# Kernel optimization log

Hardware: AMD Instinct MI355X
Metric: run time of the kernel (lower is better)

The kernel has to match this reference:

```python
import jax, jax.numpy as jnp
import numpy as np

BN_EPS = 1e-5
N_LAYERS = 3


def _mlp_bn(h, w1, b1, g, beta, w2, b2):
    # Linear -> BatchNorm1d (batch stats, training-mode math) -> ReLU -> Linear
    h = h @ w1 + b1
    mu = jnp.mean(h, axis=0)
    var = jnp.var(h, axis=0)
    h = (h - mu) * jax.lax.rsqrt(var + BN_EPS) * g + beta
    h = jax.nn.relu(h)
    return h @ w2 + b2


def setup_inputs() -> dict:
    key = jax.random.key(0)
    ks = jax.random.split(key, 20)
    N, E, XD, ED, H, C, G = 50000, 640000, 64, 16, 128, 10, 512
    L = N_LAYERS
    s = lambda fan: 1.0 / np.sqrt(fan)
    inp = {
        "x": jax.random.normal(ks[0], (N, XD), jnp.float32),
        "edge_attr": jax.random.normal(ks[1], (E, ED), jnp.float32),
        "node_w": jax.random.uniform(ks[2], (XD, H), jnp.float32, -s(XD), s(XD)),
        "node_b": jnp.zeros((H,), jnp.float32),
        "edge_w": jax.random.uniform(ks[3], (ED, H), jnp.float32, -s(ED), s(ED)),
        "edge_b": jnp.zeros((H,), jnp.float32),
        "lin1_w": jax.random.uniform(ks[4], (L, H, H), jnp.float32, -s(H), s(H)),
        "lin1_b": jnp.zeros((L, H), jnp.float32),
        "bn_g": jnp.ones((L, H), jnp.float32),
        "bn_b": jnp.zeros((L, H), jnp.float32),
        "lin2_w": jax.random.uniform(ks[5], (L, H, H), jnp.float32, -s(H), s(H)),
        "lin2_b": jnp.zeros((L, H), jnp.float32),
        "fc_w": jax.random.uniform(ks[6], (H, C), jnp.float32, -s(H), s(H)),
        "fc_b": jnp.zeros((C,), jnp.float32),
        "edge_index": jax.random.randint(ks[7], (2, E), 0, N, jnp.int64),
        "batch": jnp.sort(jax.random.randint(ks[8], (N,), 0, G, jnp.int64)),
        "num_graphs": G,
    }
    return inp


def reference(x, edge_attr, node_w, node_b, edge_w, edge_b, lin1_w, lin1_b,
              bn_g, bn_b, lin2_w, lin2_b, fc_w, fc_b, edge_index, batch, num_graphs):
    N = x.shape[0]
    src, dst = edge_index[0], edge_index[1]
    h = x @ node_w + node_b                      # [N, H] node encoder
    e = edge_attr @ edge_w + edge_b              # [E, H] edge encoder
    for i in range(N_LAYERS):
        # GINEConv: msg = relu(h[src] + e); aggr = segment_sum at dst; out = MLP(h + aggr) (eps=0)
        msg = jax.nn.relu(h[src] + e)            # [E, H]
        aggr = jax.ops.segment_sum(msg, dst, num_segments=N)
        h = _mlp_bn(h + aggr, lin1_w[i], lin1_b[i], bn_g[i], bn_b[i], lin2_w[i], lin2_b[i])
        h = jax.nn.relu(h)                       # dropout p=0 -> identity
    pooled = jax.ops.segment_sum(h, batch, num_segments=num_graphs)  # global_add_pool
    return pooled @ fc_w + fc_b
```

## Files before the change

kernel.cpp:

```cpp
#include <hip/hip_runtime.h>

#define H   128

typedef __attribute__((ext_vector_type(8))) short short8;
typedef __attribute__((ext_vector_type(4))) float f32x4;

__device__ __forceinline__ unsigned int bfr(float f) {
  unsigned int u = __float_as_uint(f);
  return (u + 0x7fffu + ((u >> 16) & 1u)) >> 16;
}
__device__ __forceinline__ float bf_lo(unsigned int d) {
  return __uint_as_float(d << 16);
}
__device__ __forceinline__ float bf_hi(unsigned int d) {
  return __uint_as_float(d & 0xffff0000u);
}

__global__ __launch_bounds__(256) void prep(const int* __restrict__ dst,
    int* __restrict__ cnt, int E, const float* __restrict__ x,
    const float* __restrict__ node_w, const float* __restrict__ node_b,
    unsigned int* __restrict__ h2, int N, const float* __restrict__ lin1_w,
    const float* __restrict__ lin2_w, unsigned short* __restrict__ wp) {
  int gtid = blockIdx.x * 256 + threadIdx.x;
  int GT = gridDim.x * 256;
  for (int e = gtid; e < E; e += GT) atomicAdd(&cnt[dst[e]], 1);
  int lane = threadIdx.x & 63;
  int wg = blockIdx.x * 4 + (threadIdx.x >> 6);
  int NW = gridDim.x * 4;
  int c = lane * 2;
  float b0 = node_b[c], b1 = node_b[c + 1];
  for (int row = wg; row < N; row += NW) {
    const float* xr = x + (size_t)row * 64;
    float a0 = b0, a1 = b1;
#pragma unroll 8
    for (int k = 0; k < 64; ++k) {
      float xk = xr[k];
      float2 wv = *(const float2*)&node_w[k * H + c];
      a0 = fmaf(xk, wv.x, a0);
      a1 = fmaf(xk, wv.y, a1);
    }
    h2[(size_t)row * 64 + lane] = bfr(a0) | (bfr(a1) << 16);
  }
  for (int idx = gtid; idx < 6 * 16384; idx += GT) {
    int j = idx & 7, ln = (idx >> 3) & 63, ct = (idx >> 9) & 7;
    int kt = (idx >> 12) & 3, mat = idx >> 14;
    int l = mat >> 1, which = mat & 1;
    const float* w = (which == 0 ? lin1_w : lin2_w) + (size_t)l * H * H;
    int k = kt * 32 + (ln >> 4) * 8 + j;
    int n = ct * 16 + (ln & 15);
    wp[idx] = (unsigned short)bfr(w[k * H + n]);
  }
}

__global__ __launch_bounds__(256) void block_sum(const int* __restrict__ cnt,
    int* __restrict__ bsum, int N) {
  int t = threadIdx.x;
  int i = blockIdx.x * 256 + t;
  int v = (i < N) ? cnt[i] : 0;
#pragma unroll
  for (int o = 32; o > 0; o >>= 1) v += __shfl_down(v, o, 64);
  __shared__ int wt[4];
  if ((t & 63) == 0) wt[t >> 6] = v;
  __syncthreads();
  if (t == 0) bsum[blockIdx.x] = wt[0] + wt[1] + wt[2] + wt[3];
}

__global__ __launch_bounds__(1024) void scan_bsum(const int* __restrict__ bsum,
    int* __restrict__ bbase, int nb) {
  __shared__ int s[1024];
  int t = threadIdx.x;
  int v = (t < nb) ? bsum[t] : 0;
  s[t] = v;
  __syncthreads();
  for (int o = 1; o < 1024; o <<= 1) {
    int u = (t >= o) ? s[t - o] : 0;
    __syncthreads();
    s[t] += u;
    __syncthreads();
  }
  if (t < nb) bbase[t] = s[t] - v;
}

__global__ __launch_bounds__(256) void scan_pass(const int* __restrict__ cnt,
    const int* __restrict__ bbase, int* __restrict__ off,
    int* __restrict__ cursor, int N) {
  int t = threadIdx.x;
  int i = blockIdx.x * 256 + t;
  int v = (i < N) ? cnt[i] : 0;
  int lane = t & 63;
  int incl = v;
#pragma unroll
  for (int o = 1; o < 64; o <<= 1) {
    int u = __shfl_up(incl, o, 64);
    if (lane >= o) incl += u;
  }
  __shared__ int wtot[4];
  int w = t >> 6;
  if (lane == 63) wtot[w] = incl;
  __syncthreads();
  if (t == 0) {
    int run = 0;
#pragma unroll
    for (int k = 0; k < 4; ++k) { int tmp = wtot[k]; wtot[k] = run; run += tmp; }
  }
  __syncthreads();
  int excl = incl - v + wtot[w] + bbase[blockIdx.x];
  if (i < N) { off[i] = excl; cursor[i] = excl; }
  if (i == N - 1) off[N] = excl + v;
}

__global__ __launch_bounds__(256) void scatter_csr(const int* __restrict__ src,
    const int* __restrict__ dst, int* __restrict__ cursor,
    int2* __restrict__ es, int E) {
  int e = blockIdx.x * 256 + threadIdx.x;
  if (e < E) {
    int pos = atomicAdd(&cursor[dst[e]], 1);
    es[pos] = make_int2(e, src[e]);
  }
}

__global__ __launch_bounds__(256) void aggr_csr(const float* __restrict__ ea,
    const float* __restrict__ ew, const float* __restrict__ eb,
    const int2* __restrict__ es, const int* __restrict__ off,
    const unsigned int* __restrict__ h2, unsigned int* __restrict__ zb,
    int N) {
  int wid = threadIdx.x >> 6, lane = threadIdx.x & 63;
  int n = blockIdx.x * 4 + wid;
  if (n >= N) return;
  int beg = off[n], end = off[n + 1];
  int c = lane * 2;
  float2 wc[16];
#pragma unroll
  for (int k = 0; k < 16; ++k) wc[k] = *(const float2*)&ew[k * H + c];
  float2 bias = *(const float2*)&eb[c];
  float ax = 0.f, ay = 0.f;
  int i = beg;
  for (; i + 4 <= end; i += 4) {
    int2 p0 = es[i], p1 = es[i + 1], p2 = es[i + 2], p3 = es[i + 3];
    int e0 = __builtin_amdgcn_readfirstlane(p0.x);
    int s0 = __builtin_amdgcn_readfirstlane(p0.y);
    int e1 = __builtin_amdgcn_readfirstlane(p1.x);
    int s1 = __builtin_amdgcn_readfirstlane(p1.y);
    int e2 = __builtin_amdgcn_readfirstlane(p2.x);
    int s2 = __builtin_amdgcn_readfirstlane(p2.y);
    int e3 = __builtin_amdgcn_readfirstlane(p3.x);
    int s3 = __builtin_amdgcn_readfirstlane(p3.y);
    unsigned int hv0 = h2[(size_t)s0 * 64 + lane];
    unsigned int hv1 = h2[(size_t)s1 * 64 + lane];
    unsigned int hv2 = h2[(size_t)s2 * 64 + lane];
    unsigned int hv3 = h2[(size_t)s3 * 64 + lane];
    const float* a0 = ea + (size_t)e0 * 16;
    const float* a1 = ea + (size_t)e1 * 16;
    const float* a2 = ea + (size_t)e2 * 16;
    const float* a3 = ea + (size_t)e3 * 16;
    float x0 = bias.x, y0 = bias.y, x1 = bias.x, y1 = bias.y;
    float x2 = bias.x, y2 = bias.y, x3 = bias.x, y3 = bias.y;
#pragma unroll
    for (int k = 0; k < 16; ++k) {
      float a0k = a0[k], a1k = a1[k], a2k = a2[k], a3k = a3[k];
      float2 w = wc[k];
      x0 = fmaf(a0k, w.x, x0); y0 = fmaf(a0k, w.y, y0);
      x1 = fmaf(a1k, w.x, x1); y1 = fmaf(a1k, w.y, y1);
      x2 = fmaf(a2k, w.x, x2); y2 = fmaf(a2k, w.y, y2);
      x3 = fmaf(a3k, w.x, x3); y3 = fmaf(a3k, w.y, y3);
    }
    ax += fmaxf(x0 + bf_lo(hv0), 0.f) + fmaxf(x1 + bf_lo(hv1), 0.f) +
          fmaxf(x2 + bf_lo(hv2), 0.f) + fmaxf(x3 + bf_lo(hv3), 0.f);
    ay += fmaxf(y0 + bf_hi(hv0), 0.f) + fmaxf(y1 + bf_hi(hv1), 0.f) +
          fmaxf(y2 + bf_hi(hv2), 0.f) + fmaxf(y3 + bf_hi(hv3), 0.f);
  }
  for (; i < end; ++i) {
    int2 p0 = es[i];
    int e0 = __builtin_amdgcn_readfirstlane(p0.x);
    int s0 = __builtin_amdgcn_readfirstlane(p0.y);
    unsigned int hv0 = h2[(size_t)s0 * 64 + lane];
    const float* a0 = ea + (size_t)e0 * 16;
    float x0 = bias.x, y0 = bias.y;
#pragma unroll
    for (int k = 0; k < 16; ++k) {
      float a0k = a0[k];
      x0 = fmaf(a0k, wc[k].x, x0);
      y0 = fmaf(a0k, wc[k].y, y0);
    }
    ax += fmaxf(x0 + bf_lo(hv0), 0.f);
    ay += fmaxf(y0 + bf_hi(hv0), 0.f);
  }
  unsigned int hn = h2[(size_t)n * 64 + lane];
  zb[(size_t)n * 64 + lane] =
      bfr(bf_lo(hn) + ax) | (bfr(bf_hi(hn) + ay) << 16);
}

__global__ __launch_bounds__(256) void mlp1m(const unsigned short* __restrict__ zb,
    const unsigned short* __restrict__ wp, const float* __restrict__ b1,
    float* __restrict__ tout, float* __restrict__ sum,
    float* __restrict__ sumsq, int N) {
  int tid = threadIdx.x;
  int wave = tid >> 6, lane = tid & 63;
  int q = lane >> 4, m = lane & 15;
  int r0 = blockIdx.x * 64 + wave * 16;
  f32x4 acc[8];
#pragma unroll
  for (int ct = 0; ct < 8; ++ct) acc[ct] = (f32x4){0.f, 0.f, 0.f, 0.f};
#pragma unroll
  for (int kt = 0; kt < 4; ++kt) {
    short8 a = *(const short8*)(zb + (size_t)(r0 + m) * H + kt * 32 + q * 8);
#pragma unroll
    for (int ct = 0; ct < 8; ++ct) {
      short8 b = *(const short8*)(wp + ((size_t)(kt * 8 + ct) * 64 + lane) * 8);
      acc[ct] = __builtin_amdgcn_mfma_f32_16x16x32_bf16(a, b, acc[ct], 0, 0, 0);
    }
  }
  __shared__ float red[2][H][16];
  int wq = wave * 4 + q;
#pragma unroll
  for (int ct = 0; ct < 8; ++ct) {
    int col = ct * 16 + m;
    float bias = b1[col];
    float s1 = 0.f, s2 = 0.f;
#pragma unroll
    for (int r = 0; r < 4; ++r) {
      int gr = r0 + q * 4 + r;
      float v = acc[ct][r] + bias;
      if (gr < N) {
        tout[(size_t)gr * H + col] = v;
        s1 += v;
        s2 += v * v;
      }
    }
    red[0][col][wq] = s1;
    red[1][col][wq] = s2;
  }
  __syncthreads();
  if (tid < H) {
    float a = 0.f, b = 0.f;
#pragma unroll
    for (int g = 0; g < 16; ++g) {
      a += red[0][tid][g];
      b += red[1][tid][g];
    }
    atomicAdd(&sum[tid], a);
    atomicAdd(&sumsq[tid], b);
  }
}

__global__ __launch_bounds__(256) void mlp2m(const float* __restrict__ tin,
    const float* __restrict__ sums, const float* __restrict__ sumsqs,
    const float* __restrict__ bng, const float* __restrict__ bnb,
    const unsigned short* __restrict__ wp, const float* __restrict__ b2,
    unsigned short* __restrict__ hout, int N, float invN,
    const int* __restrict__ batch, float* __restrict__ pooled) {
  int tid = threadIdx.x;
  __shared__ float scs[H], shs[H];
  if (tid < H) {
    float mu = sums[tid] * invN;
    float var = sumsqs[tid] * invN - mu * mu;
    float inv = rsqrtf(var + 1e-5f);
    float sc = bng[tid] * inv;
    scs[tid] = sc;
    shs[tid] = bnb[tid] - mu * sc;
  }
  __syncthreads();
  int wave = tid >> 6, lane = tid & 63;
  int q = lane >> 4, m = lane & 15;
  int r0 = blockIdx.x * 64 + wave * 16;
  int row = r0 + m;
  f32x4 acc[8];
#pragma unroll
  for (int ct = 0; ct < 8; ++ct) acc[ct] = (f32x4){0.f, 0.f, 0.f, 0.f};
#pragma unroll
  for (int kt = 0; kt < 4; ++kt) {
    int c0 = kt * 32 + q * 8;
    f32x4 t0 = *(const f32x4*)(tin + (size_t)row * H + c0);
    f32x4 t1 = *(const f32x4*)(tin + (size_t)row * H + c0 + 4);
    short8 a;
#pragma unroll
    for (int j = 0; j < 4; ++j) {
      float v = fmaxf(fmaf(t0[j], scs[c0 + j], shs[c0 + j]), 0.f);
      a[j] = (short)bfr(v);
    }
#pragma unroll
    for (int j = 0; j < 4; ++j) {
      float v = fmaxf(fmaf(t1[j], scs[c0 + 4 + j], shs[c0 + 4 + j]), 0.f);
      a[4 + j] = (short)bfr(v);
    }
#pragma unroll
    for (int ct = 0; ct < 8; ++ct) {
      short8 b = *(const short8*)(wp + ((size_t)(kt * 8 + ct) * 64 + lane) * 8);
      acc[ct] = __builtin_amdgcn_mfma_f32_16x16x32_bf16(a, b, acc[ct], 0, 0, 0);
    }
  }
#pragma unroll
  for (int ct = 0; ct < 8; ++ct) {
    float bias = b2[ct * 16 + m];
#pragma unroll
    for (int r = 0; r < 4; ++r) acc[ct][r] = fmaxf(acc[ct][r] + bias, 0.f);
  }
  if (hout != nullptr) {
#pragma unroll
    for (int r = 0; r < 4; ++r) {
      int gr = r0 + q * 4 + r;
      if (gr < N) {
#pragma unroll
        for (int ct = 0; ct < 8; ++ct)
          hout[(size_t)gr * H + ct * 16 + m] = (unsigned short)bfr(acc[ct][r]);
      }
    }
  }
  if (pooled != nullptr) {
    int bprev = -1;
    float pa[8];
#pragma unroll
    for (int ct = 0; ct < 8; ++ct) pa[ct] = 0.f;
    for (int r = 0; r < 4; ++r) {
      int gr = r0 + q * 4 + r;
      if (gr >= N) break;
      int bb = batch[gr];
      if (bb != bprev && bprev >= 0) {
#pragma unroll
        for (int ct = 0; ct < 8; ++ct) {
          atomicAdd(&pooled[(size_t)bprev * H + ct * 16 + m], pa[ct]);
          pa[ct] = 0.f;
        }
      }
      bprev = bb;
#pragma unroll
      for (int ct = 0; ct < 8; ++ct) pa[ct] += acc[ct][r];
    }
    if (bprev >= 0) {
#pragma unroll
      for (int ct = 0; ct < 8; ++ct)
        atomicAdd(&pooled[(size_t)bprev * H + ct * 16 + m], pa[ct]);
    }
  }
}

__global__ __launch_bounds__(128) void fc_kernel(const float* __restrict__ pooled,
    const float* __restrict__ w, const float* __restrict__ b,
    float* __restrict__ out, int C) {
  int g = blockIdx.x;
  int j = threadIdx.x;
  __shared__ float p[H];
  p[j] = pooled[(size_t)g * H + j];
  __syncthreads();
  if (j < C) {
    float acc = b[j];
#pragma unroll 4
    for (int k = 0; k < H; ++k) acc = fmaf(p[k], w[k * C + j], acc);
    out[(size_t)g * C + j] = acc;
  }
}

extern "C" void kernel_launch(void* const* d_in, const int* in_sizes, int n_in,
                              void* d_out, int out_size, void* d_ws, size_t ws_size,
                              hipStream_t stream) {
  const float* x         = (const float*)d_in[0];
  const float* edge_attr = (const float*)d_in[1];
  const float* node_w    = (const float*)d_in[2];
  const float* node_b    = (const float*)d_in[3];
  const float* edge_w    = (const float*)d_in[4];
  const float* edge_b    = (const float*)d_in[5];
  const float* lin1_w    = (const float*)d_in[6];
  const float* lin1_b    = (const float*)d_in[7];
  const float* bn_g      = (const float*)d_in[8];
  const float* bn_b      = (const float*)d_in[9];
  const float* lin2_w    = (const float*)d_in[10];
  const float* lin2_b    = (const float*)d_in[11];
  const float* fc_w      = (const float*)d_in[12];
  const float* fc_b      = (const float*)d_in[13];
  const int*   edge_index= (const int*)d_in[14];
  const int*   batch     = (const int*)d_in[15];

  int N = in_sizes[0] / 64;
  int E = in_sizes[1] / 16;
  int C = in_sizes[13];
  int G = out_size / C;

  const int* src = edge_index;
  const int* dst = edge_index + E;

  int mblk = (N + 63) / 64;
  int Npad = mblk * 64;
  int nb = (N + 255) / 256;

  float* t      = (float*)d_ws;
  float* pooled = t + (size_t)Npad * H;
  float* sumsA  = pooled + (size_t)G * H;
  int*   cnt    = (int*)(sumsA + 3 * 256);
  size_t zbytes = ((size_t)G * H + 3 * 256 + N) * 4;
  int*   off    = cnt + N;
  int*   cursor = off + N + 2;
  int2*  es     = (int2*)(cursor + N);
  unsigned int* h2 = (unsigned int*)(es + E);
  unsigned int* zb = h2 + (size_t)Npad * 64;
  unsigned short* wp = (unsigned short*)(zb + (size_t)Npad * 64);
  int* bsum  = (int*)(wp + 6 * 16384);
  int* bbase = bsum + 1024;

  hipMemsetAsync(pooled, 0, zbytes, stream);
  prep<<<1024, 256, 0, stream>>>(dst, cnt, E, x, node_w, node_b, h2, N,
                                 lin1_w, lin2_w, wp);
  block_sum<<<nb, 256, 0, stream>>>(cnt, bsum, N);
  scan_bsum<<<1, 1024, 0, stream>>>(bsum, bbase, nb);
  scan_pass<<<nb, 256, 0, stream>>>(cnt, bbase, off, cursor, N);
  scatter_csr<<<(E + 255) / 256, 256, 0, stream>>>(src, dst, cursor, es, E);

  int ablk = (N + 3) / 4;
  for (int l = 0; l < 3; ++l) {
    aggr_csr<<<ablk, 256, 0, stream>>>(edge_attr, edge_w, edge_b, es, off,
                                       h2, zb, N);
    mlp1m<<<mblk, 256, 0, stream>>>((const unsigned short*)zb,
                                    wp + (size_t)(l * 2) * 16384,
                                    lin1_b + (size_t)l * H, t,
                                    sumsA + l * 256, sumsA + l * 256 + 128, N);
    bool last = (l == 2);
    mlp2m<<<mblk, 256, 0, stream>>>(t, sumsA + l * 256, sumsA + l * 256 + 128,
                                    bn_g + (size_t)l * H, bn_b + (size_t)l * H,
                                    wp + (size_t)(l * 2 + 1) * 16384,
                                    lin2_b + (size_t)l * H,
                                    last ? nullptr : (unsigned short*)h2, N,
                                    1.0f / N, batch, last ? pooled : nullptr);
  }

  fc_kernel<<<G, 128, 0, stream>>>(pooled, fc_w, fc_b, (float*)d_out, C);
}
```

Measured before the change: 670.1 us.

## Store pre-BN activations as bf16 and split prep into separate kernels

The intermediate MLP activation buffer between mlp1m and mlp2m is now written and read as bf16 instead of fp32, halving that round-trip traffic on each of the three layers. The fused prep kernel is also split into three kernels: degree counting, a per-row node encoder that stages x in shared memory, and weight packing. BN statistics are still accumulated in fp32 before rounding, but normalising bf16-rounded values adds some precision loss. The split also adds two launches.

```diff
diff --git a/kernel.cpp b/kernel.cpp
--- a/kernel.cpp
+++ b/kernel.cpp
@@ -16,40 +16,42 @@
   return __uint_as_float(d & 0xffff0000u);
 }
 
-__global__ __launch_bounds__(256) void prep(const int* __restrict__ dst,
-    int* __restrict__ cnt, int E, const float* __restrict__ x,
-    const float* __restrict__ node_w, const float* __restrict__ node_b,
-    unsigned int* __restrict__ h2, int N, const float* __restrict__ lin1_w,
-    const float* __restrict__ lin2_w, unsigned short* __restrict__ wp) {
-  int gtid = blockIdx.x * 256 + threadIdx.x;
-  int GT = gridDim.x * 256;
-  for (int e = gtid; e < E; e += GT) atomicAdd(&cnt[dst[e]], 1);
-  int lane = threadIdx.x & 63;
-  int wg = blockIdx.x * 4 + (threadIdx.x >> 6);
-  int NW = gridDim.x * 4;
-  int c = lane * 2;
-  float b0 = node_b[c], b1 = node_b[c + 1];
-  for (int row = wg; row < N; row += NW) {
-    const float* xr = x + (size_t)row * 64;
-    float a0 = b0, a1 = b1;
-#pragma unroll 8
-    for (int k = 0; k < 64; ++k) {
-      float xk = xr[k];
-      float2 wv = *(const float2*)&node_w[k * H + c];
-      a0 = fmaf(xk, wv.x, a0);
-      a1 = fmaf(xk, wv.y, a1);
-    }
-    h2[(size_t)row * 64 + lane] = bfr(a0) | (bfr(a1) << 16);
-  }
-  for (int idx = gtid; idx < 6 * 16384; idx += GT) {
-    int j = idx & 7, ln = (idx >> 3) & 63, ct = (idx >> 9) & 7;
-    int kt = (idx >> 12) & 3, mat = idx >> 14;
-    int l = mat >> 1, which = mat & 1;
-    const float* w = (which == 0 ? lin1_w : lin2_w) + (size_t)l * H * H;
-    int k = kt * 32 + (ln >> 4) * 8 + j;
-    int n = ct * 16 + (ln & 15);
-    wp[idx] = (unsigned short)bfr(w[k * H + n]);
-  }
+__global__ __launch_bounds__(128) void node_enc(const float* __restrict__ x,
+    const float* __restrict__ w, const float* __restrict__ b,
+    unsigned int* __restrict__ h2, int N) {
+  int row = blockIdx.x;
+  if (row >= N) return;
+  int j = threadIdx.x;
+  __shared__ float xs[64];
+  if (j < 64) xs[j] = x[(size_t)row * 64 + j];
+  __syncthreads();
+  float acc = b[j];
+#pragma unroll
+  for (int k = 0; k < 64; ++k) acc = fmaf(xs[k], w[k * H + j], acc);
+  float part = __shfl_down(acc, 1, 64);
+  if ((j & 1) == 0) {
+    unsigned int d = bfr(acc) | (bfr(part) << 16);
+    h2[(size_t)row * 64 + (j >> 1)] = d;
+  }
+}
+
+__global__ __launch_bounds__(256) void count_deg(const int* __restrict__ dst,
+    int* __restrict__ cnt, int E) {
+  int e = blockIdx.x * 256 + threadIdx.x;
+  if (e < E) atomicAdd(&cnt[dst[e]], 1);
+}
+
+__global__ __launch_bounds__(256) void wpack(const float* __restrict__ w1,
+    const float* __restrict__ w2, unsigned short* __restrict__ wp) {
+  int idx = blockIdx.x * 256 + threadIdx.x;
+  if (idx >= 6 * 16384) return;
+  int j = idx & 7, ln = (idx >> 3) & 63, ct = (idx >> 9) & 7;
+  int kt = (idx >> 12) & 3, mat = idx >> 14;
+  int l = mat >> 1, which = mat & 1;
+  const float* w = (which == 0 ? w1 : w2) + (size_t)l * H * H;
+  int k = kt * 32 + (ln >> 4) * 8 + j;
+  int n = ct * 16 + (ln & 15);
+  wp[idx] = (unsigned short)bfr(w[k * H + n]);
 }
 
 __global__ __launch_bounds__(256) void block_sum(const int* __restrict__ cnt,
@@ -192,7 +194,7 @@
 
 __global__ __launch_bounds__(256) void mlp1m(const unsigned short* __restrict__ zb,
     const unsigned short* __restrict__ wp, const float* __restrict__ b1,
-    float* __restrict__ tout, float* __restrict__ sum,
+    unsigned short* __restrict__ tout, float* __restrict__ sum,
     float* __restrict__ sumsq, int N) {
   int tid = threadIdx.x;
   int wave = tid >> 6, lane = tid & 63;
@@ -222,7 +224,7 @@
       int gr = r0 + q * 4 + r;
       float v = acc[ct][r] + bias;
       if (gr < N) {
-        tout[(size_t)gr * H + col] = v;
+        tout[(size_t)gr * H + col] = (unsigned short)bfr(v);
         s1 += v;
         s2 += v * v;
       }
@@ -243,7 +245,7 @@
   }
 }
 
-__global__ __launch_bounds__(256) void mlp2m(const float* __restrict__ tin,
+__global__ __launch_bounds__(256) void mlp2m(const unsigned short* __restrict__ tin,
     const float* __restrict__ sums, const float* __restrict__ sumsqs,
     const float* __restrict__ bng, const float* __restrict__ bnb,
     const unsigned short* __restrict__ wp, const float* __restrict__ b2,
@@ -270,19 +272,17 @@
 #pragma unroll
   for (int kt = 0; kt < 4; ++kt) {
     int c0 = kt * 32 + q * 8;
-    f32x4 t0 = *(const f32x4*)(tin + (size_t)row * H + c0);
-    f32x4 t1 = *(const f32x4*)(tin + (size_t)row * H + c0 + 4);
+    uint4 tv = *(const uint4*)(tin + (size_t)row * H + c0);
     short8 a;
-#pragma unroll
-    for (int j = 0; j < 4; ++j) {
-      float v = fmaxf(fmaf(t0[j], scs[c0 + j], shs[c0 + j]), 0.f);
-      a[j] = (short)bfr(v);
-    }
-#pragma unroll
-    for (int j = 0; j < 4; ++j) {
-      float v = fmaxf(fmaf(t1[j], scs[c0 + 4 + j], shs[c0 + 4 + j]), 0.f);
-      a[4 + j] = (short)bfr(v);
-    }
+    float v;
+    v = fmaxf(fmaf(bf_lo(tv.x), scs[c0 + 0], shs[c0 + 0]), 0.f); a[0] = (short)bfr(v);
+    v = fmaxf(fmaf(bf_hi(tv.x), scs[c0 + 1], shs[c0 + 1]), 0.f); a[1] = (short)bfr(v);
+    v = fmaxf(fmaf(bf_lo(tv.y), scs[c0 + 2], shs[c0 + 2]), 0.f); a[2] = (short)bfr(v);
+    v = fmaxf(fmaf(bf_hi(tv.y), scs[c0 + 3], shs[c0 + 3]), 0.f); a[3] = (short)bfr(v);
+    v = fmaxf(fmaf(bf_lo(tv.z), scs[c0 + 4], shs[c0 + 4]), 0.f); a[4] = (short)bfr(v);
+    v = fmaxf(fmaf(bf_hi(tv.z), scs[c0 + 5], shs[c0 + 5]), 0.f); a[5] = (short)bfr(v);
+    v = fmaxf(fmaf(bf_lo(tv.w), scs[c0 + 6], shs[c0 + 6]), 0.f); a[6] = (short)bfr(v);
+    v = fmaxf(fmaf(bf_hi(tv.w), scs[c0 + 7], shs[c0 + 7]), 0.f); a[7] = (short)bfr(v);
 #pragma unroll
     for (int ct = 0; ct < 8; ++ct) {
       short8 b = *(const short8*)(wp + ((size_t)(kt * 8 + ct) * 64 + lane) * 8);
@@ -382,8 +382,8 @@
   int Npad = mblk * 64;
   int nb = (N + 255) / 256;
 
-  float* t      = (float*)d_ws;
-  float* pooled = t + (size_t)Npad * H;
+  unsigned short* t = (unsigned short*)d_ws;
+  float* pooled = (float*)(t + (size_t)Npad * H);
   float* sumsA  = pooled + (size_t)G * H;
   int*   cnt    = (int*)(sumsA + 3 * 256);
   size_t zbytes = ((size_t)G * H + 3 * 256 + N) * 4;
@@ -397,8 +397,9 @@
   int* bbase = bsum + 1024;
 
   hipMemsetAsync(pooled, 0, zbytes, stream);
-  prep<<<1024, 256, 0, stream>>>(dst, cnt, E, x, node_w, node_b, h2, N,
-                                 lin1_w, lin2_w, wp);
+  count_deg<<<(E + 255) / 256, 256, 0, stream>>>(dst, cnt, E);
+  node_enc<<<N, 128, 0, stream>>>(x, node_w, node_b, h2, N);
+  wpack<<<(6 * 16384 + 255) / 256, 256, 0, stream>>>(lin1_w, lin2_w, wp);
   block_sum<<<nb, 256, 0, stream>>>(cnt, bsum, N);
   scan_bsum<<<1, 1024, 0, stream>>>(bsum, bbase, nb);
   scan_pass<<<nb, 256, 0, stream>>>(cnt, bbase, off, cursor, N);
```

Result: faster. 605.2 us (-9.7%).
